# Optimization experiments

Measured on AMD Instinct MI355X. Metric: run time of the kernel, lower is better.

## Reference

```python
import jax, jax.numpy as jnp
import numpy as np
from jax import lax

PATCH = 3  # match_patch_size
EPS = 1e-9
WEIGHT = 100.0


def _patches(fm, p):
    # fm: [1, C, H, W] -> sliding p x p patches with reflect pad -> [H*W, C*p*p]
    pad = (p - 1) // 2
    fm_pad = jnp.pad(fm, ((0, 0), (0, 0), (pad, pad), (pad, pad)), mode='reflect')
    pt = lax.conv_general_dilated_patches(fm_pad, (p, p), (1, 1), 'VALID')  # [1, C*p*p, H, W]
    _, cpp, H, W = pt.shape
    return pt.reshape(cpp, H * W).T  # [H*W, C*p*p]


def _match_fm(content_fm, style_fm, p):
    # normalized cross-correlation patch match; returns matched style fm [1,C,H,W]
    _, C, H, W = content_fm.shape
    cp = _patches(content_fm, p)           # [HW, Cpp]
    sp = _patches(style_fm, p)             # [HW, Cpp]
    cn = jnp.sqrt(jnp.sum(cp * cp, axis=1))  # [HW]
    sn = jnp.sqrt(jnp.sum(sp * sp, axis=1))  # [HW]
    score = cp @ sp.T                       # [HW, HW] dense correlation
    score = score / (cn[:, None] * sn[None, :] + EPS)
    idx = jnp.argmax(score, axis=1)         # best style location per content location
    y, x = idx // W, idx % W
    corr = style_fm[0, :, y, x]             # [HW, C] gather
    return corr.T.reshape(1, C, H, W)


def _gram(fm):
    # fm: [B, C, H, W] -> [B, C, C]
    B, C, H, W = fm.shape
    f = fm.reshape(B, C, H * W)
    return jnp.einsum('bcx,bdx->bcd', f, f)


def setup_inputs() -> dict:
    key = jax.random.key(0)
    k1, k2, k3, k4 = jax.random.split(key, 4)
    shape = (1, 256, 64, 64)
    return {
        'content_fm': jax.random.normal(k1, shape, dtype=jnp.float32),
        'style_fm': jax.random.normal(k2, shape, dtype=jnp.float32),
        'input_fm': jax.random.normal(k3, shape, dtype=jnp.float32),
        'mask': jax.random.uniform(k4, (1, 1, 64, 64), dtype=jnp.float32),
    }


def reference(content_fm, style_fm, input_fm, mask):
    mask_exp = jnp.broadcast_to(mask, content_fm.shape)
    msum = jnp.sum(mask_exp)
    # capture_style phase: patch match + masked target gram
    corr = _match_fm(content_fm, style_fm, PATCH)
    target = lax.stop_gradient(_gram(corr * mask_exp) / msum)
    # loss phase
    G = _gram(input_fm * mask_exp) / msum
    loss = jnp.mean((G - target) ** 2) * WEIGHT
    return loss
```

## Files before the change

### kernel.cpp

```cpp
#include <hip/hip_runtime.h>
#include <math.h>

#define C_CH 256
#define NPOS 4096
#define PAD_W 66
#define PAD_HW (PAD_W*PAD_W)
#define GSLICE 32
#define CHUNK 8

typedef __bf16 bf16x8 __attribute__((ext_vector_type(8)));
typedef float  f32x4  __attribute__((ext_vector_type(4)));

__device__ __forceinline__ int reflect_idx(int p) {
    int s = p - 1;
    if (s < 0) s = -s;
    if (s > 63) s = 126 - s;
    return s;
}

__device__ __forceinline__ unsigned short f2bf(float x) {
    unsigned int u = __float_as_uint(x);
    unsigned int r = u + 0x7fffu + ((u >> 16) & 1u);
    return (unsigned short)(r >> 16);
}

__device__ __forceinline__ unsigned int fmono(float f) {
    unsigned int b = __float_as_uint(f);
    return (b & 0x80000000u) ? ~b : (b | 0x80000000u);
}

__device__ __forceinline__ void gload16(const void* g, void* l) {
    __builtin_amdgcn_global_load_lds(
        (const __attribute__((address_space(1))) unsigned int*)g,
        (__attribute__((address_space(3))) unsigned int*)l, 16, 0, 0);
}

__global__ void __launch_bounds__(256)
split_kernel(const float* __restrict__ content, const float* __restrict__ style,
             unsigned short* __restrict__ cTH, unsigned short* __restrict__ cTL,
             unsigned short* __restrict__ sTH, unsigned short* __restrict__ sTL,
             float* __restrict__ SSp) {
    __shared__ float tile[64][65];
    int t = threadIdx.x;

    if (blockIdx.z == 2) {
        int bi = blockIdx.y * 69 + blockIdx.x;
        if (bi >= 128) return;
        int pos = ((bi & 15) << 8) + t;
        int cg = bi >> 4;
        float s = 0.f;
        for (int c = cg * 32; c < cg * 32 + 32; ++c) {
            float v = style[(size_t)c * NPOS + pos];
            s += v * v;
        }
        SSp[cg * NPOS + pos] = s;
        return;
    }

    const float* src = blockIdx.z ? style : content;
    unsigned short* oH = blockIdx.z ? sTH : cTH;
    unsigned short* oL = blockIdx.z ? sTL : cTL;
    int p0 = blockIdx.x * 64, c0 = blockIdx.y * 64;
    int posl = t & 63;
    int p = p0 + posl; int pc = p < PAD_HW ? p : PAD_HW - 1;
    int py = pc / PAD_W, px = pc - py * PAD_W;
    int rawIdx = reflect_idx(py) * 64 + reflect_idx(px);
    #pragma unroll
    for (int r = 0; r < 16; ++r) {
        int cl = (t >> 6) + r * 4;
        tile[posl][cl] = src[(size_t)(c0 + cl) * NPOS + rawIdx];
    }
    __syncthreads();
    int cl2 = t & 63;
    #pragma unroll
    for (int r = 0; r < 16; ++r) {
        int pl = (t >> 6) + r * 4;
        int pg = p0 + pl;
        if (pg < PAD_HW) {
            float x = tile[pl][cl2];
            unsigned short h = f2bf(x);
            float hf = __uint_as_float((unsigned int)h << 16);
            unsigned short l = f2bf(x - hf);
            oH[(size_t)pg * C_CH + c0 + cl2] = h;
            oL[(size_t)pg * C_CH + c0 + cl2] = l;
        }
    }
}

__global__ void __launch_bounds__(512, 4)
egemm_mfma(const unsigned short* __restrict__ AH, const unsigned short* __restrict__ AL,
           const unsigned short* __restrict__ BH, const unsigned short* __restrict__ BL,
           float* __restrict__ E,
           const float* __restrict__ SSp, float* __restrict__ rs,
           unsigned long long* __restrict__ PK,
           int colBaseQ, int colLim, int Ncols, int gx, int nwg) {
    __shared__ short sm[32768];

    int orig = blockIdx.x;
    int t = threadIdx.x;

    if (orig < 8) {
        int j = (orig << 9) + t;
        int yj = j >> 6, xj = j & 63;
        float s = 0.f;
        #pragma unroll
        for (int kh = 0; kh < 3; ++kh) {
            int ry = reflect_idx(yj + kh);
            #pragma unroll
            for (int kw = 0; kw < 3; ++kw) {
                int p = ry * 64 + reflect_idx(xj + kw);
                #pragma unroll
                for (int part = 0; part < 8; ++part)
                    s += SSp[part * NPOS + p];
            }
        }
        rs[j] = 1.0f / sqrtf(s);
        PK[j] = 0ull;
        asm volatile("s_waitcnt vmcnt(0)" ::: "memory");
    }

    int q = nwg >> 3, r = nwg & 7;
    int xcd = orig & 7, rank = orig >> 3;
    int L = (xcd < r ? xcd * (q + 1) : r * (q + 1) + (xcd - r) * q) + rank;
    int by = L / gx, bx = L - by * gx;

    int lane = t & 63, wv = t >> 6;
    int wr = wv >> 2, wc = wv & 3;
    int bm = by * 128, bn = bx * 128;
    int rowLoc = lane >> 2;
    int kc2 = (((lane & 3) ^ ((lane >> 3) & 3))) << 3;
    int krd = (((lane >> 4) ^ ((lane >> 1) & 3))) << 3;

    const unsigned short* mats[4] = {AH, AL, BH, BL};
    const unsigned short* M = mats[wv >> 1];
    int rbase = ((wv >> 1) >= 2 ? colBaseQ + bn : bm) + (wv & 1) * 64;
    const unsigned short* gp[4];
    #pragma unroll
    for (int i = 0; i < 4; ++i) {
        int rr = rbase + i * 16 + rowLoc;
        if (rr > PAD_HW - 1) rr = PAD_HW - 1;
        gp[i] = M + (size_t)rr * C_CH + kc2;
    }
    int ldst = wv * 2048;

    auto STAGE = [&](short* base, int koff) {
        #pragma unroll
        for (int i = 0; i < 4; ++i)
            gload16(gp[i] + koff, base + ldst + i * 512);
    };

    f32x4 acc[4][2];
    #pragma unroll
    for (int mt = 0; mt < 4; ++mt)
        #pragma unroll
        for (int nt = 0; nt < 2; ++nt)
            acc[mt][nt] = (f32x4){0.f, 0.f, 0.f, 0.f};

    STAGE(sm, 0);

    #pragma unroll
    for (int ks = 0; ks < 8; ++ks) {
        short* cb = sm + (ks & 1) * 16384;
        if (ks < 7) {
            STAGE(sm + ((ks + 1) & 1) * 16384, (ks + 1) * 32);
            asm volatile("s_waitcnt vmcnt(4)" ::: "memory");
        } else {
            asm volatile("s_waitcnt vmcnt(0)" ::: "memory");
        }
        __builtin_amdgcn_s_barrier();
        __builtin_amdgcn_sched_barrier(0);

        short* sAH = cb;
        short* sAL = cb + 4096;
        short* sBH = cb + 8192;
        short* sBL = cb + 12288;
        bf16x8 aH[4], aL[4], bH[2], bL[2];
        #pragma unroll
        for (int mt = 0; mt < 4; ++mt) {
            int off = (wr * 64 + mt * 16 + (lane & 15)) * 32 + krd;
            aH[mt] = *(const bf16x8*)(sAH + off);
            aL[mt] = *(const bf16x8*)(sAL + off);
        }
        #pragma unroll
        for (int nt = 0; nt < 2; ++nt) {
            int off = (wc * 32 + nt * 16 + (lane & 15)) * 32 + krd;
            bH[nt] = *(const bf16x8*)(sBH + off);
            bL[nt] = *(const bf16x8*)(sBL + off);
        }
        __builtin_amdgcn_s_setprio(1);
        #pragma unroll
        for (int mt = 0; mt < 4; ++mt)
            #pragma unroll
            for (int nt = 0; nt < 2; ++nt) {
                f32x4 c = acc[mt][nt];
                c = __builtin_amdgcn_mfma_f32_16x16x32_bf16(aH[mt], bH[nt], c, 0, 0, 0);
                c = __builtin_amdgcn_mfma_f32_16x16x32_bf16(aH[mt], bL[nt], c, 0, 0, 0);
                c = __builtin_amdgcn_mfma_f32_16x16x32_bf16(aL[mt], bH[nt], c, 0, 0, 0);
                acc[mt][nt] = c;
            }
        __builtin_amdgcn_s_setprio(0);

        asm volatile("s_waitcnt lgkmcnt(0)" ::: "memory");
        __builtin_amdgcn_s_barrier();
        __builtin_amdgcn_sched_barrier(0);
    }

    #pragma unroll
    for (int mt = 0; mt < 4; ++mt) {
        int row0 = bm + wr * 64 + mt * 16 + (lane >> 4) * 4;
        #pragma unroll
        for (int nt = 0; nt < 2; ++nt) {
            int col = bn + wc * 32 + nt * 16 + (lane & 15);
            if (col < colLim) {
                #pragma unroll
                for (int r2 = 0; r2 < 4; ++r2) {
                    int row = row0 + r2;
                    if (row < PAD_HW)
                        E[(size_t)row * Ncols + col] = acc[mt][nt][r2];
                }
            }
        }
    }
}

__global__ void __launch_bounds__(256)
score_argmax(const float* __restrict__ E, const float* __restrict__ rs,
             unsigned long long* __restrict__ PK,
             int g, int R, int Ncols) {
    __shared__ float T[3 * 66 * 68];
    __shared__ float sv[4][64];
    __shared__ int   sj[4][64];

    int bid = blockIdx.x;
    int d = bid % R;
    int c = bid / R;
    int s0 = c * CHUNK;
    int t = threadIdx.x;
    int xi = t & 63, s2 = t >> 6, xj0 = s2 * 16;

    int u0 = t / 66, v0 = t - u0 * 66;

    bool valid = false;
    float r[18];

    for (int s = s0; s < s0 + CHUNK; ++s) {
        int yjl = (s + d) & (R - 1);

        if (!valid) {
            __syncthreads();
            for (int kh = 0; kh < 3; ++kh) {
                float* Tb = T + ((s + kh) % 3) * 4488;
                const float* Eb = E + (size_t)((s + kh) * 66) * Ncols + (yjl + kh) * 66;
                int u = u0, v = v0;
                #pragma unroll
                for (int i = 0; i < 17; ++i) {
                    Tb[u * 68 + v] = Eb[(size_t)u * Ncols + v];
                    v += 58; u += 3; if (v >= 66) { v -= 66; ++u; }
                }
                if (t < 4) Tb[65 * 68 + 62 + t] = Eb[(size_t)65 * Ncols + 62 + t];
            }
            __syncthreads();
            valid = true;
        }

        int yjl_next = (s + 1 + d) & (R - 1);
        bool pf = (s + 1 < s0 + CHUNK) && (yjl_next == yjl + 1);
        if (pf) {
            const float* Eb = E + (size_t)((s + 3) * 66) * Ncols + (yjl + 3) * 66;
            int u = u0, v = v0;
            #pragma unroll
            for (int i = 0; i < 17; ++i) {
                r[i] = Eb[(size_t)u * Ncols + v];
                v += 58; u += 3; if (v >= 66) { v -= 66; ++u; }
            }
            if (t < 4) r[17] = Eb[(size_t)65 * Ncols + 62 + t];
        }

        float sc[16];
        #pragma unroll
        for (int q2 = 0; q2 < 16; ++q2) sc[q2] = 0.f;
        #pragma unroll
        for (int kh = 0; kh < 3; ++kh) {
            const float* Tk = T + ((s + kh) % 3) * 4488;
            #pragma unroll
            for (int kw = 0; kw < 3; ++kw) {
                const float* rp = Tk + (xi + kw) * 68 + xj0;
                float rr[18];
                *(float4*)&rr[0]  = *(const float4*)&rp[0];
                *(float4*)&rr[4]  = *(const float4*)&rp[4];
                *(float4*)&rr[8]  = *(const float4*)&rp[8];
                *(float4*)&rr[12] = *(const float4*)&rp[12];
                if (kw > 0) *(float2*)&rr[16] = *(const float2*)&rp[16];
                #pragma unroll
                for (int q2 = 0; q2 < 16; ++q2) sc[q2] += rr[kw + q2];
            }
        }

        int jbase = ((g * R + yjl) << 6) + xj0;
        float bv = -INFINITY; int bj = 0;
        #pragma unroll
        for (int q2 = 0; q2 < 16; ++q2) {
            float v = sc[q2] * rs[jbase + q2];
            if (v > bv) { bv = v; bj = jbase + q2; }
        }
        sv[s2][xi] = bv; sj[s2][xi] = bj;
        __syncthreads();
        if (s2 == 0) {
            #pragma unroll
            for (int u = 1; u < 4; ++u) {
                float ov = sv[u][xi]; int oj = sj[u][xi];
                if (ov > bv || (ov == bv && oj < bj)) { bv = ov; bj = oj; }
            }
            unsigned long long pk =
                ((unsigned long long)fmono(bv) << 32) | (unsigned int)(~bj);
            atomicMax(PK + (s << 6) + xi, pk);
        }

        if (pf) {
            __syncthreads();
            float* Tb = T + ((s + 3) % 3) * 4488;
            int u = u0, v = v0;
            #pragma unroll
            for (int i = 0; i < 17; ++i) {
                Tb[u * 68 + v] = r[i];
                v += 58; u += 3; if (v >= 66) { v -= 66; ++u; }
            }
            if (t < 4) Tb[65 * 68 + 62 + t] = r[17];
            __syncthreads();
        } else {
            valid = false;
        }
    }
}

__global__ void __launch_bounds__(256)
build_xy_kernel(const float* __restrict__ input_fm,
                const float* __restrict__ style,
                const float* __restrict__ mask,
                const unsigned long long* __restrict__ PK,
                unsigned short* __restrict__ XmH, unsigned short* __restrict__ XmL,
                unsigned short* __restrict__ YmH, unsigned short* __restrict__ YmL,
                float* __restrict__ out) {
    if (blockIdx.x == 0 && threadIdx.x == 0) *out = 0.0f;
    int e4 = blockIdx.x * 256 + threadIdx.x;
    int c = e4 >> 10;
    int i0 = (e4 & 1023) << 2;
    int base = (c << 12) + i0;
    float4 inv = *(const float4*)&input_fm[base];
    float4 mv  = *(const float4*)&mask[i0];
    const float* sc = style + ((size_t)c << 12);
    float x[4], y[4];
    x[0] = inv.x * mv.x; x[1] = inv.y * mv.y; x[2] = inv.z * mv.z; x[3] = inv.w * mv.w;
    float mvv[4] = {mv.x, mv.y, mv.z, mv.w};
    #pragma unroll
    for (int k = 0; k < 4; ++k) {
        unsigned long long pk = PK[i0 + k];
        int j = (int)(~(unsigned int)(pk & 0xffffffffu));
        y[k] = sc[j] * mvv[k];
    }
    ushort4 xh, xl, yh, yl;
    #pragma unroll
    for (int j = 0; j < 4; ++j) {
        unsigned short h = f2bf(x[j]);
        float hf = __uint_as_float((unsigned int)h << 16);
        ((unsigned short*)&xh)[j] = h;
        ((unsigned short*)&xl)[j] = f2bf(x[j] - hf);
        unsigned short h2 = f2bf(y[j]);
        float hf2 = __uint_as_float((unsigned int)h2 << 16);
        ((unsigned short*)&yh)[j] = h2;
        ((unsigned short*)&yl)[j] = f2bf(y[j] - hf2);
    }
    *(ushort4*)&XmH[base] = xh;
    *(ushort4*)&XmL[base] = xl;
    *(ushort4*)&YmH[base] = yh;
    *(ushort4*)&YmL[base] = yl;
}

__global__ void __launch_bounds__(256)
gram_mfma(const unsigned short* __restrict__ XH, const unsigned short* __restrict__ XL,
          const unsigned short* __restrict__ YH, const unsigned short* __restrict__ YL,
          float* __restrict__ Dpart) {
    __shared__ short sm[32768];
    const int PI[10] = {0,0,0,0,1,1,1,2,2,3};
    const int PJ[10] = {0,1,2,3,1,2,3,2,3,3};
    int pr = blockIdx.x, sl = blockIdx.y;
    int ti = PI[pr], tj = PJ[pr];
    int c0 = ti * 64, d0 = tj * 64;
    int t = threadIdx.x, lane = t & 63, wv = t >> 6;
    int wr = wv >> 1, wc = wv & 1;
    int rowLoc = wv * 16 + (lane >> 2);
    int kc2 = (((lane & 3) ^ ((lane >> 3) & 3))) << 3;
    int krd = (((lane >> 4) ^ ((lane >> 1) & 3))) << 3;
    int posBase = sl * 128 + kc2;

    const unsigned short* g0 = XH + (size_t)(c0 + rowLoc) * NPOS + posBase;
    const unsigned short* g1 = XL + (size_t)(c0 + rowLoc) * NPOS + posBase;
    const unsigned short* g2 = XH + (size_t)(d0 + rowLoc) * NPOS + posBase;
    const unsigned short* g3 = XL + (size_t)(d0 + rowLoc) * NPOS + posBase;
    const unsigned short* g4 = YH + (size_t)(c0 + rowLoc) * NPOS + posBase;
    const unsigned short* g5 = YL + (size_t)(c0 + rowLoc) * NPOS + posBase;
    const unsigned short* g6 = YH + (size_t)(d0 + rowLoc) * NPOS + posBase;
    const unsigned short* g7 = YL + (size_t)(d0 + rowLoc) * NPOS + posBase;
    int lb = wv * 512;

    auto STAGE = [&](short* base, int koff) {
        gload16(g0 + koff, base + lb);
        gload16(g1 + koff, base + 2048 + lb);
        gload16(g2 + koff, base + 4096 + lb);
        gload16(g3 + koff, base + 6144 + lb);
        gload16(g4 + koff, base + 8192 + lb);
        gload16(g5 + koff, base + 10240 + lb);
        gload16(g6 + koff, base + 12288 + lb);
        gload16(g7 + koff, base + 14336 + lb);
    };

    f32x4 aX[2][2], aY[2][2];
    #pragma unroll
    for (int mt = 0; mt < 2; ++mt)
        #pragma unroll
        for (int nt = 0; nt < 2; ++nt) {
            aX[mt][nt] = (f32x4){0.f, 0.f, 0.f, 0.f};
            aY[mt][nt] = (f32x4){0.f, 0.f, 0.f, 0.f};
        }

    STAGE(sm, 0);

    #pragma unroll
    for (int ks = 0; ks < 4; ++ks) {
        short* cb = sm + (ks & 1) * 16384;
        if (ks < 3) {
            STAGE(sm + ((ks + 1) & 1) * 16384, (ks + 1) * 32);
            asm volatile("s_waitcnt vmcnt(8)" ::: "memory");
        } else {
            asm volatile("s_waitcnt vmcnt(0)" ::: "memory");
        }
        __builtin_amdgcn_s_barrier();
        __builtin_amdgcn_sched_barrier(0);

        bf16x8 xcH[2], xcL[2], xdH[2], xdL[2], ycH[2], ycL[2], ydH[2], ydL[2];
        #pragma unroll
        for (int mt = 0; mt < 2; ++mt) {
            int off = (wr * 32 + mt * 16 + (lane & 15)) * 32 + krd;
            xcH[mt] = *(const bf16x8*)(cb + off);
            xcL[mt] = *(const bf16x8*)(cb + 2048 + off);
            ycH[mt] = *(const bf16x8*)(cb + 8192 + off);
            ycL[mt] = *(const bf16x8*)(cb + 10240 + off);
        }
        #pragma unroll
        for (int nt = 0; nt < 2; ++nt) {
            int off = (wc * 32 + nt * 16 + (lane & 15)) * 32 + krd;
            xdH[nt] = *(const bf16x8*)(cb + 4096 + off);
            xdL[nt] = *(const bf16x8*)(cb + 6144 + off);
            ydH[nt] = *(const bf16x8*)(cb + 12288 + off);
            ydL[nt] = *(const bf16x8*)(cb + 14336 + off);
        }
        __builtin_amdgcn_s_setprio(1);
        #pragma unroll
        for (int mt = 0; mt < 2; ++mt)
            #pragma unroll
            for (int nt = 0; nt < 2; ++nt) {
                f32x4 cx = aX[mt][nt];
                cx = __builtin_amdgcn_mfma_f32_16x16x32_bf16(xcH[mt], xdH[nt], cx, 0, 0, 0);
                cx = __builtin_amdgcn_mfma_f32_16x16x32_bf16(xcH[mt], xdL[nt], cx, 0, 0, 0);
                cx = __builtin_amdgcn_mfma_f32_16x16x32_bf16(xcL[mt], xdH[nt], cx, 0, 0, 0);
                aX[mt][nt] = cx;
                f32x4 cy = aY[mt][nt];
                cy = __builtin_amdgcn_mfma_f32_16x16x32_bf16(ycH[mt], ydH[nt], cy, 0, 0, 0);
                cy = __builtin_amdgcn_mfma_f32_16x16x32_bf16(ycH[mt], ydL[nt], cy, 0, 0, 0);
                cy = __builtin_amdgcn_mfma_f32_16x16x32_bf16(ycL[mt], ydH[nt], cy, 0, 0, 0);
                aY[mt][nt] = cy;
            }
        __builtin_amdgcn_s_setprio(0);

        asm volatile("s_waitcnt lgkmcnt(0)" ::: "memory");
        __builtin_amdgcn_s_barrier();
        __builtin_amdgcn_sched_barrier(0);
    }

    float* fs = (float*)sm;
    #pragma unroll
    for (int mt = 0; mt < 2; ++mt) {
        int rl = wr * 32 + mt * 16 + ((lane >> 4) << 2);
        #pragma unroll
        for (int nt = 0; nt < 2; ++nt) {
            int cl = wc * 32 + nt * 16 + (lane & 15);
            #pragma unroll
            for (int r2 = 0; r2 < 4; ++r2)
                fs[(rl + r2) * 68 + cl] = aX[mt][nt][r2] - aY[mt][nt][r2];
        }
    }
    __syncthreads();
    float* Db = Dpart + ((size_t)sl * 10 + pr) * 4096;
    int rr0 = t >> 4;
    int cc0 = (t & 15) << 2;
    #pragma unroll
    for (int i = 0; i < 4; ++i) {
        int rr = rr0 + (i << 4);
        *(float4*)&Db[rr * 64 + cc0] = *(const float4*)&fs[rr * 68 + cc0];
    }
}

__global__ void __launch_bounds__(256)
loss_kernel(const float* __restrict__ Dpart, const float* __restrict__ mask,
            float* __restrict__ out) {
    const int PI[10] = {0,0,0,0,1,1,1,2,2,3};
    const int PJ[10] = {0,1,2,3,1,2,3,2,3,3};
    __shared__ float red[4];
    int tid = threadIdx.x;

    float ms = 0.f;
    for (int i = tid; i < NPOS; i += 256) ms += mask[i];
    #pragma unroll
    for (int o = 32; o >= 1; o >>= 1) ms += __shfl_down(ms, o, 64);
    if ((tid & 63) == 0) red[tid >> 6] = ms;
    __syncthreads();
    float msum = 256.0f * (red[0] + red[1] + red[2] + red[3]);
    __syncthreads();

    int e2 = blockIdx.x * 256 + tid;
    int tt = e2 >> 12;
    int ei = e2 & 4095;
    float d = 0.f;
    #pragma unroll
    for (int s = 0; s < GSLICE; ++s)
        d += Dpart[(size_t)(s * 10 + tt) * 4096 + ei];
    float inv = 1.0f / msum;
    float v = d * inv;
    float w = (PI[tt] != PJ[tt]) ? 2.0f : 1.0f;
    float ls = w * v * v;
    #pragma unroll
    for (int o = 32; o >= 1; o >>= 1) ls += __shfl_down(ls, o, 64);
    if ((tid & 63) == 0) red[tid >> 6] = ls;
    __syncthreads();
    if (tid == 0)
        atomicAdd(out, (red[0] + red[1] + red[2] + red[3]) * (100.0f / 65536.0f));
}

extern "C" void kernel_launch(void* const* d_in, const int* in_sizes, int n_in,
                              void* d_out, int out_size, void* d_ws, size_t ws_size,
                              hipStream_t stream) {
    (void)in_sizes; (void)n_in; (void)out_size;
    const float* content = (const float*)d_in[0];
    const float* style   = (const float*)d_in[1];
    const float* input   = (const float*)d_in[2];
    const float* mask    = (const float*)d_in[3];
    float* out = (float*)d_out;

    auto alignup = [](size_t b) { return (b + 255) & ~size_t(255); };

    size_t szT   = alignup((size_t)PAD_HW * C_CH * 2);
    size_t szSS  = alignup((size_t)8 * NPOS * 4);
    size_t szRS  = alignup((size_t)NPOS * 4);
    size_t szPK  = alignup((size_t)NPOS * 8);
    size_t szXYb = alignup((size_t)C_CH * NPOS * 2);
    size_t szDp  = alignup((size_t)GSLICE * 10 * 4096 * 4);
    size_t fixed = 4 * szT + szSS + szRS + szPK + 4 * szXYb + szDp;

    auto padcols = [](int c) { return (c + 15) & ~15; };

    auto needE = [&](int NG) {
        size_t Nc = (size_t)padcols((64 / NG + 2) * PAD_W);
        return fixed + alignup((size_t)PAD_HW * Nc * 4) + 4096;
    };
    int NG = 8;
    if      (ws_size >= needE(1)) NG = 1;
    else if (ws_size >= needE(2)) NG = 2;
    else if (ws_size >= needE(4)) NG = 4;
    int R = 64 / NG;
    int colLim = (R + 2) * PAD_W;
    int Ncols = padcols(colLim);

    char* ws = (char*)d_ws;
    size_t off = 0;
    auto alloc = [&](size_t bytes) { void* p = ws + off; off += alignup(bytes); return p; };

    unsigned short* cTH = (unsigned short*)alloc((size_t)PAD_HW * C_CH * 2);
    unsigned short* cTL = (unsigned short*)alloc((size_t)PAD_HW * C_CH * 2);
    unsigned short* sTH = (unsigned short*)alloc((size_t)PAD_HW * C_CH * 2);
    unsigned short* sTL = (unsigned short*)alloc((size_t)PAD_HW * C_CH * 2);
    float* SSp   = (float*)alloc((size_t)8 * NPOS * 4);
    float* rs    = (float*)alloc((size_t)NPOS * 4);
    unsigned long long* PK = (unsigned long long*)alloc((size_t)NPOS * 8);
    unsigned short* XmH = (unsigned short*)alloc((size_t)C_CH * NPOS * 2);
    unsigned short* XmL = (unsigned short*)alloc((size_t)C_CH * NPOS * 2);
    unsigned short* YmH = (unsigned short*)alloc((size_t)C_CH * NPOS * 2);
    unsigned short* YmL = (unsigned short*)alloc((size_t)C_CH * NPOS * 2);
    float* Dpart = (float*)alloc((size_t)GSLICE * 10 * 4096 * 4);
    float* E     = (float*)alloc((size_t)PAD_HW * Ncols * 4);

    split_kernel<<<dim3(69, 4, 3), 256, 0, stream>>>(content, style, cTH, cTL, sTH, sTL, SSp);

    int gx = (colLim + 127) / 128;
    int gy = (PAD_HW + 127) / 128;
    int nwg = gx * gy;
    for (int g = 0; g < NG; ++g) {
        int colBaseQ = g * R * PAD_W;
        egemm_mfma<<<nwg, 512, 0, stream>>>(cTH, cTL, sTH, sTL, E, SSp, rs, PK,
                                            colBaseQ, colLim, Ncols, gx, nwg);
        score_argmax<<<R * (64 / CHUNK), 256, 0, stream>>>(E, rs, PK, g, R, Ncols);
    }
    build_xy_kernel<<<1024, 256, 0, stream>>>(input, style, mask, PK, XmH, XmL, YmH, YmL, out);
    gram_mfma<<<dim3(10, GSLICE), 256, 0, stream>>>(XmH, XmL, YmH, YmL, Dpart);
    loss_kernel<<<160, 256, 0, stream>>>(Dpart, mask, out);
}
```

Before: 109.2 us.

## Compute correlation GEMM on unpadded 64x64 grid, apply reflection in score stage

After: 101.7 us (median of 2 runs). -6.9%, faster.

```diff
diff --git a/kernel.cpp b/kernel.cpp
--- a/kernel.cpp
+++ b/kernel.cpp
@@ -3,10 +3,9 @@
 
 #define C_CH 256
 #define NPOS 4096
-#define PAD_W 66
-#define PAD_HW (PAD_W*PAD_W)
 #define GSLICE 32
 #define CHUNK 8
+#define ENC 4112
 
 typedef __bf16 bf16x8 __attribute__((ext_vector_type(8)));
 typedef float  f32x4  __attribute__((ext_vector_type(4)));
@@ -44,7 +43,7 @@
     int t = threadIdx.x;
 
     if (blockIdx.z == 2) {
-        int bi = blockIdx.y * 69 + blockIdx.x;
+        int bi = blockIdx.y * 64 + blockIdx.x;
         if (bi >= 128) return;
         int pos = ((bi & 15) << 8) + t;
         int cg = bi >> 4;
@@ -62,13 +61,11 @@
     unsigned short* oL = blockIdx.z ? sTL : cTL;
     int p0 = blockIdx.x * 64, c0 = blockIdx.y * 64;
     int posl = t & 63;
-    int p = p0 + posl; int pc = p < PAD_HW ? p : PAD_HW - 1;
-    int py = pc / PAD_W, px = pc - py * PAD_W;
-    int rawIdx = reflect_idx(py) * 64 + reflect_idx(px);
+    int p = p0 + posl;
     #pragma unroll
     for (int r = 0; r < 16; ++r) {
         int cl = (t >> 6) + r * 4;
-        tile[posl][cl] = src[(size_t)(c0 + cl) * NPOS + rawIdx];
+        tile[posl][cl] = src[(size_t)(c0 + cl) * NPOS + p];
     }
     __syncthreads();
     int cl2 = t & 63;
@@ -76,14 +73,12 @@
     for (int r = 0; r < 16; ++r) {
         int pl = (t >> 6) + r * 4;
         int pg = p0 + pl;
-        if (pg < PAD_HW) {
-            float x = tile[pl][cl2];
-            unsigned short h = f2bf(x);
-            float hf = __uint_as_float((unsigned int)h << 16);
-            unsigned short l = f2bf(x - hf);
-            oH[(size_t)pg * C_CH + c0 + cl2] = h;
-            oL[(size_t)pg * C_CH + c0 + cl2] = l;
-        }
+        float x = tile[pl][cl2];
+        unsigned short h = f2bf(x);
+        float hf = __uint_as_float((unsigned int)h << 16);
+        unsigned short l = f2bf(x - hf);
+        oH[(size_t)pg * C_CH + c0 + cl2] = h;
+        oL[(size_t)pg * C_CH + c0 + cl2] = l;
     }
 }
 
@@ -92,8 +87,7 @@
            const unsigned short* __restrict__ BH, const unsigned short* __restrict__ BL,
            float* __restrict__ E,
            const float* __restrict__ SSp, float* __restrict__ rs,
-           unsigned long long* __restrict__ PK,
-           int colBaseQ, int colLim, int Ncols, int gx, int nwg) {
+           unsigned long long* __restrict__ PK, int nwg) {
     __shared__ short sm[32768];
 
     int orig = blockIdx.x;
@@ -119,10 +113,10 @@
         asm volatile("s_waitcnt vmcnt(0)" ::: "memory");
     }
 
-    int q = nwg >> 3, r = nwg & 7;
+    int q = nwg >> 3;
     int xcd = orig & 7, rank = orig >> 3;
-    int L = (xcd < r ? xcd * (q + 1) : r * (q + 1) + (xcd - r) * q) + rank;
-    int by = L / gx, bx = L - by * gx;
+    int L = xcd * q + rank;
+    int by = L >> 5, bx = L & 31;
 
     int lane = t & 63, wv = t >> 6;
     int wr = wv >> 2, wc = wv & 3;
@@ -133,14 +127,11 @@
 
     const unsigned short* mats[4] = {AH, AL, BH, BL};
     const unsigned short* M = mats[wv >> 1];
-    int rbase = ((wv >> 1) >= 2 ? colBaseQ + bn : bm) + (wv & 1) * 64;
+    int rbase = ((wv >> 1) >= 2 ? bn : bm) + (wv & 1) * 64;
     const unsigned short* gp[4];
     #pragma unroll
-    for (int i = 0; i < 4; ++i) {
-        int rr = rbase + i * 16 + rowLoc;
-        if (rr > PAD_HW - 1) rr = PAD_HW - 1;
-        gp[i] = M + (size_t)rr * C_CH + kc2;
-    }
+    for (int i = 0; i < 4; ++i)
+        gp[i] = M + (size_t)(rbase + i * 16 + rowLoc) * C_CH + kc2;
     int ldst = wv * 2048;
 
     auto STAGE = [&](short* base, int koff) {
@@ -211,69 +202,77 @@
         #pragma unroll
         for (int nt = 0; nt < 2; ++nt) {
             int col = bn + wc * 32 + nt * 16 + (lane & 15);
-            if (col < colLim) {
-                #pragma unroll
-                for (int r2 = 0; r2 < 4; ++r2) {
-                    int row = row0 + r2;
-                    if (row < PAD_HW)
-                        E[(size_t)row * Ncols + col] = acc[mt][nt][r2];
-                }
-            }
+            #pragma unroll
+            for (int r2 = 0; r2 < 4; ++r2)
+                E[(size_t)(row0 + r2) * ENC + col] = acc[mt][nt][r2];
         }
     }
 }
 
 __global__ void __launch_bounds__(256)
 score_argmax(const float* __restrict__ E, const float* __restrict__ rs,
-             unsigned long long* __restrict__ PK,
-             int g, int R, int Ncols) {
+             unsigned long long* __restrict__ PK) {
     __shared__ float T[3 * 66 * 68];
     __shared__ float sv[4][64];
     __shared__ int   sj[4][64];
 
     int bid = blockIdx.x;
-    int d = bid % R;
-    int c = bid / R;
+    int d = bid & 63;
+    int c = bid >> 6;
     int s0 = c * CHUNK;
     int t = threadIdx.x;
     int xi = t & 63, s2 = t >> 6, xj0 = s2 * 16;
-
-    int u0 = t / 66, v0 = t - u0 * 66;
+    int rr = t >> 2;
+    int j0 = (t & 3) << 4;
+
+    auto STORESTRIP = [&](float* Tb, const float* w) {
+        float* row = Tb + (rr + 1) * 68;
+        #pragma unroll
+        for (int q2 = 0; q2 < 16; ++q2) row[1 + j0 + q2] = w[q2];
+        if (j0 == 0)  row[0]  = w[1];
+        if (j0 == 48) row[65] = w[14];
+        if (rr == 1 || rr == 62) {
+            float* erow = Tb + (rr == 1 ? 0 : 65) * 68;
+            #pragma unroll
+            for (int q2 = 0; q2 < 16; ++q2) erow[1 + j0 + q2] = w[q2];
+            if (j0 == 0)  erow[0]  = w[1];
+            if (j0 == 48) erow[65] = w[14];
+        }
+    };
+    auto LOADSTRIP = [&](float* Tb, int cy, int sy) {
+        int cyr = reflect_idx(cy), syr = reflect_idx(sy);
+        const float* Eb = E + (size_t)(cyr * 64 + rr) * ENC + syr * 64 + j0;
+        float w[16];
+        *(float4*)&w[0]  = *(const float4*)&Eb[0];
+        *(float4*)&w[4]  = *(const float4*)&Eb[4];
+        *(float4*)&w[8]  = *(const float4*)&Eb[8];
+        *(float4*)&w[12] = *(const float4*)&Eb[12];
+        STORESTRIP(Tb, w);
+    };
 
     bool valid = false;
-    float r[18];
+    float pfv[16];
 
     for (int s = s0; s < s0 + CHUNK; ++s) {
-        int yjl = (s + d) & (R - 1);
+        int yjl = (s + d) & 63;
 
         if (!valid) {
             __syncthreads();
-            for (int kh = 0; kh < 3; ++kh) {
-                float* Tb = T + ((s + kh) % 3) * 4488;
-                const float* Eb = E + (size_t)((s + kh) * 66) * Ncols + (yjl + kh) * 66;
-                int u = u0, v = v0;
-                #pragma unroll
-                for (int i = 0; i < 17; ++i) {
-                    Tb[u * 68 + v] = Eb[(size_t)u * Ncols + v];
-                    v += 58; u += 3; if (v >= 66) { v -= 66; ++u; }
-                }
-                if (t < 4) Tb[65 * 68 + 62 + t] = Eb[(size_t)65 * Ncols + 62 + t];
-            }
+            for (int kh = 0; kh < 3; ++kh)
+                LOADSTRIP(T + ((s + kh) % 3) * 4488, s + kh, yjl + kh);
             __syncthreads();
             valid = true;
         }
 
-        int yjl_next = (s + 1 + d) & (R - 1);
+        int yjl_next = (s + 1 + d) & 63;
         bool pf = (s + 1 < s0 + CHUNK) && (yjl_next == yjl + 1);
         if (pf) {
-            const float* Eb = E + (size_t)((s + 3) * 66) * Ncols + (yjl + 3) * 66;
-            int u = u0, v = v0;
-            #pragma unroll
-            for (int i = 0; i < 17; ++i) {
-                r[i] = Eb[(size_t)u * Ncols + v];
-                v += 58; u += 3; if (v >= 66) { v -= 66; ++u; }
-            }
-            if (t < 4) r[17] = Eb[(size_t)65 * Ncols + 62 + t];
+            int cyr = reflect_idx(s + 3), syr = reflect_idx(yjl + 3);
+            const float* Eb = E + (size_t)(cyr * 64 + rr) * ENC + syr * 64 + j0;
+            *(float4*)&pfv[0]  = *(const float4*)&Eb[0];
+            *(float4*)&pfv[4]  = *(const float4*)&Eb[4];
+            *(float4*)&pfv[8]  = *(const float4*)&Eb[8];
+            *(float4*)&pfv[12] = *(const float4*)&Eb[12];
         }
 
         float sc[16];
@@ -285,18 +284,18 @@
             #pragma unroll
             for (int kw = 0; kw < 3; ++kw) {
                 const float* rp = Tk + (xi + kw) * 68 + xj0;
-                float rr[18];
-                *(float4*)&rr[0]  = *(const float4*)&rp[0];
-                *(float4*)&rr[4]  = *(const float4*)&rp[4];
-                *(float4*)&rr[8]  = *(const float4*)&rp[8];
-                *(float4*)&rr[12] = *(const float4*)&rp[12];
-                if (kw > 0) *(float2*)&rr[16] = *(const float2*)&rp[16];
+                float rw[18];
+                *(float4*)&rw[0]  = *(const float4*)&rp[0];
+                *(float4*)&rw[4]  = *(const float4*)&rp[4];
+                *(float4*)&rw[8]  = *(const float4*)&rp[8];
+                *(float4*)&rw[12] = *(const float4*)&rp[12];
+                if (kw > 0) *(float2*)&rw[16] = *(const float2*)&rp[16];
                 #pragma unroll
-                for (int q2 = 0; q2 < 16; ++q2) sc[q2] += rr[kw + q2];
+                for (int q2 = 0; q2 < 16; ++q2) sc[q2] += rw[kw + q2];
             }
         }
 
-        int jbase = ((g * R + yjl) << 6) + xj0;
+        int jbase = (yjl << 6) + xj0;
         float bv = -INFINITY; int bj = 0;
         #pragma unroll
         for (int q2 = 0; q2 < 16; ++q2) {
@@ -318,14 +317,7 @@
 
         if (pf) {
             __syncthreads();
-            float* Tb = T + ((s + 3) % 3) * 4488;
-            int u = u0, v = v0;
-            #pragma unroll
-            for (int i = 0; i < 17; ++i) {
-                Tb[u * 68 + v] = r[i];
-                v += 58; u += 3; if (v >= 66) { v -= 66; ++u; }
-            }
-            if (t < 4) Tb[65 * 68 + 62 + t] = r[17];
+            STORESTRIP(T + ((s + 3) % 3) * 4488, pfv);
             __syncthreads();
         } else {
             valid = false;
@@ -539,7 +531,7 @@
 extern "C" void kernel_launch(void* const* d_in, const int* in_sizes, int n_in,
                               void* d_out, int out_size, void* d_ws, size_t ws_size,
                               hipStream_t stream) {
-    (void)in_sizes; (void)n_in; (void)out_size;
+    (void)in_sizes; (void)n_in; (void)out_size; (void)ws_size;
     const float* content = (const float*)d_in[0];
     const float* style   = (const float*)d_in[1];
     const float* input   = (const float*)d_in[2];
@@ -547,37 +539,14 @@
     float* out = (float*)d_out;
 
     auto alignup = [](size_t b) { return (b + 255) & ~size_t(255); };
-
-    size_t szT   = alignup((size_t)PAD_HW * C_CH * 2);
-    size_t szSS  = alignup((size_t)8 * NPOS * 4);
-    size_t szRS  = alignup((size_t)NPOS * 4);
-    size_t szPK  = alignup((size_t)NPOS * 8);
-    size_t szXYb = alignup((size_t)C_CH * NPOS * 2);
-    size_t szDp  = alignup((size_t)GSLICE * 10 * 4096 * 4);
-    size_t fixed = 4 * szT + szSS + szRS + szPK + 4 * szXYb + szDp;
-
-    auto padcols = [](int c) { return (c + 15) & ~15; };
-
-    auto needE = [&](int NG) {
-        size_t Nc = (size_t)padcols((64 / NG + 2) * PAD_W);
-        return fixed + alignup((size_t)PAD_HW * Nc * 4) + 4096;
-    };
-    int NG = 8;
-    if      (ws_size >= needE(1)) NG = 1;
-    else if (ws_size >= needE(2)) NG = 2;
-    else if (ws_size >= needE(4)) NG = 4;
-    int R = 64 / NG;
-    int colLim = (R + 2) * PAD_W;
-    int Ncols = padcols(colLim);
-
     char* ws = (char*)d_ws;
     size_t off = 0;
     auto alloc = [&](size_t bytes) { void* p = ws + off; off += alignup(bytes); return p; };
 
-    unsigned short* cTH = (unsigned short*)alloc((size_t)PAD_HW * C_CH * 2);
-    unsigned short* cTL = (unsigned short*)alloc((size_t)PAD_HW * C_CH * 2);
-    unsigned short* sTH = (unsigned short*)alloc((size_t)PAD_HW * C_CH * 2);
-    unsigned short* sTL = (unsigned short*)alloc((size_t)PAD_HW * C_CH * 2);
+    unsigned short* cTH = (unsigned short*)alloc((size_t)NPOS * C_CH * 2);
+    unsigned short* cTL = (unsigned short*)alloc((size_t)NPOS * C_CH * 2);
+    unsigned short* sTH = (unsigned short*)alloc((size_t)NPOS * C_CH * 2);
+    unsigned short* sTL = (unsigned short*)alloc((size_t)NPOS * C_CH * 2);
     float* SSp   = (float*)alloc((size_t)8 * NPOS * 4);
     float* rs    = (float*)alloc((size_t)NPOS * 4);
     unsigned long long* PK = (unsigned long long*)alloc((size_t)NPOS * 8);
@@ -586,19 +555,13 @@
     unsigned short* YmH = (unsigned short*)alloc((size_t)C_CH * NPOS * 2);
     unsigned short* YmL = (unsigned short*)alloc((size_t)C_CH * NPOS * 2);
     float* Dpart = (float*)alloc((size_t)GSLICE * 10 * 4096 * 4);
-    float* E     = (float*)alloc((size_t)PAD_HW * Ncols * 4);
-
-    split_kernel<<<dim3(69, 4, 3), 256, 0, stream>>>(content, style, cTH, cTL, sTH, sTL, SSp);
-
-    int gx = (colLim + 127) / 128;
-    int gy = (PAD_HW + 127) / 128;
-    int nwg = gx * gy;
-    for (int g = 0; g < NG; ++g) {
-        int colBaseQ = g * R * PAD_W;
-        egemm_mfma<<<nwg, 512, 0, stream>>>(cTH, cTL, sTH, sTL, E, SSp, rs, PK,
-                                            colBaseQ, colLim, Ncols, gx, nwg);
-        score_argmax<<<R * (64 / CHUNK), 256, 0, stream>>>(E, rs, PK, g, R, Ncols);
-    }
+    float* E     = (float*)alloc((size_t)NPOS * ENC * 4);
+
+    split_kernel<<<dim3(64, 4, 3), 256, 0, stream>>>(content, style, cTH, cTL, sTH, sTL, SSp);
+
+    int nwg = 1024;
+    egemm_mfma<<<nwg, 512, 0, stream>>>(cTH, cTL, sTH, sTL, E, SSp, rs, PK, nwg);
+    score_argmax<<<512, 256, 0, stream>>>(E, rs, PK);
     build_xy_kernel<<<1024, 256, 0, stream>>>(input, style, mask, PK, XmH, XmL, YmH, YmL, out);
     gram_mfma<<<dim3(10, GSLICE), 256, 0, stream>>>(XmH, XmL, YmH, YmL, Dpart);
     loss_kernel<<<160, 256, 0, stream>>>(Dpart, mask, out);
```
